# Performance work log

Measured on AMD Instinct MI355X. Metric: run time of the kernel, lower is better.

Reference implementation:

```python
import jax, jax.numpy as jnp
import numpy as np

OUTPUT_LEN = 8  # init: output_len
# init: pred_conversion=False, conf_thres=None, vote_conf_by_count=True, select_by_conf=True


def setup_inputs() -> dict:
    key = jax.random.key(0)
    x = jax.random.normal(key, (128, 8192, 64), dtype=jnp.float32)
    return {"x": x}


def _per_sample(conf, pred):
    # conf, pred: [T]
    T = conf.shape[0]
    # run-length encoding (unique_consecutive): mark the start of each run
    is_start = jnp.concatenate([jnp.ones((1,), bool), pred[1:] != pred[:-1]])
    run_id = jnp.cumsum(is_start.astype(jnp.int32)) - 1  # [T], run index per position
    # count of each run (padded to T segments; unused segments are 0)
    counts = jax.ops.segment_sum(jnp.ones((T,), conf.dtype), run_id, num_segments=T)
    # voted confidence at run starts: conf_at_start * run_count (vote_conf_by_count=True)
    voted = jnp.where(is_start, conf * counts[run_id], -jnp.inf)
    # select_by_conf=True: take top output_len runs by voted confidence
    vals, idx = jax.lax.top_k(voted, OUTPUT_LEN)
    sel = pred[idx]
    # fewer runs than output_len -> pad with 0 (torch pads with new_zeros)
    sel = jnp.where(jnp.isfinite(vals), sel, 0)
    return sel


def reference(x):
    p = jax.nn.softmax(x, axis=-1)          # [B, T, C]
    conf = jnp.max(p, axis=-1)              # [B, T]
    pred = jnp.argmax(p, axis=-1)           # [B, T] int
    out = jax.vmap(_per_sample)(conf, pred)  # [B, OUTPUT_LEN] int
    return out.astype(x.dtype)               # x.new_tensor(results) -> float
```

## Files before the change

### kernel.cpp

```cpp
#include <hip/hip_runtime.h>
#include <stdint.h>

#define T_LEN 8192
#define C_LEN 64
#define OUT_LEN 8
#define SEG 2048
#define HALO 512

__global__ __launch_bounds__(256) void softmax_stats_kernel(
    const float* __restrict__ x, int2* __restrict__ packed, int nrows)
{
    const int tid  = threadIdx.x;
    const int wave = tid >> 6;
    const int lane = tid & 63;
    const int rw   = lane >> 4;
    const int sub  = lane & 15;
    const long long row = (long long)blockIdx.x * 16 + wave * 4 + rw;
    if (row >= nrows) return;

    const float4 v = ((const float4*)(x + row * C_LEN))[sub];

    float m = v.x; int mi = sub * 4;
    if (v.y > m) { m = v.y; mi = sub * 4 + 1; }
    if (v.z > m) { m = v.z; mi = sub * 4 + 2; }
    if (v.w > m) { m = v.w; mi = sub * 4 + 3; }

    const unsigned int s0 = __float_as_uint(m);
    const unsigned int u0 = (s0 & 0x80000000u) ? ~s0 : (s0 | 0x80000000u);
    unsigned long long key =
        ((unsigned long long)u0 << 32) | (unsigned int)~mi;

    #pragma unroll
    for (int off = 8; off >= 1; off >>= 1) {
        const unsigned long long o = __shfl_xor(key, off);
        if (o > key) key = o;
    }

    const unsigned int uu = (unsigned int)(key >> 32);
    const float M = __uint_as_float(
        (uu & 0x80000000u) ? (uu ^ 0x80000000u) : ~uu);

    float s = __expf(v.x - M) + __expf(v.y - M)
            + __expf(v.z - M) + __expf(v.w - M);
    #pragma unroll
    for (int off = 8; off >= 1; off >>= 1) s += __shfl_xor(s, off);

    if (sub == 0) {
        int2 o;
        o.x = __float_as_int(1.0f / s);
        o.y = (int)~(unsigned int)(key & 0xffffffffu);
        packed[row] = o;
    }
}

__global__ __launch_bounds__(256) void topk_seg_kernel(
    const int2* __restrict__ packed, unsigned long long* __restrict__ cand)
{
    __shared__ short pred_s[SEG + HALO + 1];
    __shared__ float conf_s[SEG];
    __shared__ float voted_s[SEG];
    __shared__ unsigned long long wkey[4];
    __shared__ int dirty;

    const int tid    = threadIdx.x;
    const int lane   = tid & 63, wave = tid >> 6;
    const int sample = blockIdx.x >> 2;
    const int seg    = blockIdx.x & 3;
    const int seg_start = seg * SEG;
    const int2* __restrict__ pp = packed + (long long)sample * T_LEN;

    const int lo = (seg == 0) ? 0 : seg_start - 1;
    int hi = seg_start + SEG + HALO; if (hi > T_LEN) hi = T_LEN;
    for (int i = lo + tid; i < hi; i += 256) {
        const int2 p = pp[i];
        pred_s[i - seg_start + 1] = (short)p.y;
        const int k = i - seg_start;
        if ((unsigned)k < SEG) conf_s[k] = __int_as_float(p.x);
    }
    if (seg == 0 && tid == 0) pred_s[0] = (short)0x7fff;
    if (tid == 0) dirty = -1;
    __syncthreads();

    for (int k = tid; k < SEG; k += 256) {
        const int t = seg_start + k;
        const short p = pred_s[k + 1];
        float v = 0.0f;
        if (p != pred_s[k]) {
            int len = 1;
            const int lim = hi - t;
            while (len < lim && pred_s[k + 1 + len] == p) ++len;
            if (len == lim && t + len < T_LEN) {
                while (t + len < T_LEN && (short)pp[t + len].y == p) ++len;
            }
            v = conf_s[k] * (float)len;
        }
        voted_s[k] = v;
    }
    __syncthreads();

    for (int r = 0; r < OUT_LEN; ++r) {
        if (dirty == -1 || dirty == wave) {
            unsigned long long best = 0ull;
            const int base = wave * (SEG / 4);
            #pragma unroll
            for (int kk = 0; kk < SEG / 4 / 64; ++kk) {
                const int k = base + kk * 64 + lane;
                const unsigned long long key =
                    ((unsigned long long)__float_as_uint(voted_s[k]) << 32)
                    | (unsigned int)~(seg_start + k);
                if (key > best) best = key;
            }
            #pragma unroll
            for (int off = 32; off >= 1; off >>= 1) {
                const unsigned long long o = __shfl_xor(best, off);
                if (o > best) best = o;
            }
            if (lane == 0) wkey[wave] = best;
        }
        __syncthreads();
        if (tid == 0) {
            unsigned long long bb = wkey[0];
            #pragma unroll
            for (int w = 1; w < 4; ++w) if (wkey[w] > bb) bb = wkey[w];
            if ((bb >> 32) != 0ull) {
                const int tg = (int)~(unsigned int)(bb & 0xffffffffu);
                const int k = tg - seg_start;
                voted_s[k] = 0.0f;
                dirty = k / (SEG / 4);
            } else {
                dirty = 4;
            }
            cand[(long long)blockIdx.x * OUT_LEN + r] = bb;
        }
        __syncthreads();
    }
}

__global__ __launch_bounds__(64) void topk_merge_kernel(
    const unsigned long long* __restrict__ cand,
    const int2* __restrict__ packed, float* __restrict__ out)
{
    const int sample = blockIdx.x;
    const int lane   = threadIdx.x;

    unsigned long long key = 0ull;
    float pv = 0.0f;
    if (lane < 4 * OUT_LEN) key = cand[(long long)sample * 32 + lane];
    if (key != 0ull) {
        const int tg = (int)~(unsigned int)(key & 0xffffffffu);
        pv = (float)packed[(long long)sample * T_LEN + tg].y;
    }

    for (int r = 0; r < OUT_LEN; ++r) {
        unsigned long long best = key;
        #pragma unroll
        for (int off = 32; off >= 1; off >>= 1) {
            const unsigned long long o = __shfl_xor(best, off);
            if (o > best) best = o;
        }
        if (best == 0ull) {
            if (lane == 0) out[sample * OUT_LEN + r] = 0.0f;
        } else if (key == best) {
            out[sample * OUT_LEN + r] = pv;
            key = 0ull;
        }
    }
}

extern "C" void kernel_launch(void* const* d_in, const int* in_sizes, int n_in,
                              void* d_out, int out_size, void* d_ws, size_t ws_size,
                              hipStream_t stream) {
    const float* x  = (const float*)d_in[0];
    const int total = in_sizes[0];
    const int nrows = total / C_LEN;
    const int B     = nrows / T_LEN;

    int2* packed = (int2*)d_ws;
    unsigned long long* cand =
        (unsigned long long*)((char*)d_ws + (size_t)nrows * sizeof(int2));
    float* out = (float*)d_out;

    const int gridA = (nrows + 15) / 16;
    softmax_stats_kernel<<<gridA, 256, 0, stream>>>(x, packed, nrows);
    topk_seg_kernel<<<B * 4, 256, 0, stream>>>(packed, cand);
    topk_merge_kernel<<<B, 64, 0, stream>>>(cand, packed, out);
}
```

Baseline: 353.4 us.

## Fuse segmented top-k and merge into one per-sample kernel with register sorting networks

Replaces the two-kernel segmented top-k (4 blocks per sample, 8 serial argmax rounds with barriers, then a merge kernel) with one block of 512 threads per sample. Each thread builds 16 run-start keys, keeps its top 8 with sorting networks, and then does butterfly merges across the wave and across waves. This removes the candidate buffer, one launch, and the per-round block syncs. The cost is heavy register pressure from u64 arrays and only 128 blocks in flight, so the top-k stage has lower parallelism.

```diff
diff --git a/kernel.cpp b/kernel.cpp
--- a/kernel.cpp
+++ b/kernel.cpp
@@ -4,8 +4,7 @@
 #define T_LEN 8192
 #define C_LEN 64
 #define OUT_LEN 8
-#define SEG 2048
-#define HALO 512
+#define BTHREADS 512
 
 __global__ __launch_bounds__(256) void softmax_stats_kernel(
     const float* __restrict__ x, int2* __restrict__ packed, int nrows)
@@ -53,116 +52,112 @@
     }
 }
 
-__global__ __launch_bounds__(256) void topk_seg_kernel(
-    const int2* __restrict__ packed, unsigned long long* __restrict__ cand)
+typedef unsigned long long u64k;
+
+__device__ __forceinline__ void kcswap(u64k& a, u64k& b) {
+    if (a < b) { u64k t = a; a = b; b = t; }
+}
+
+__device__ __forceinline__ void sort8(u64k* k) {
+    kcswap(k[0],k[1]); kcswap(k[2],k[3]); kcswap(k[4],k[5]); kcswap(k[6],k[7]);
+    kcswap(k[0],k[2]); kcswap(k[1],k[3]); kcswap(k[4],k[6]); kcswap(k[5],k[7]);
+    kcswap(k[1],k[2]); kcswap(k[5],k[6]);
+    kcswap(k[0],k[4]); kcswap(k[1],k[5]); kcswap(k[2],k[6]); kcswap(k[3],k[7]);
+    kcswap(k[2],k[4]); kcswap(k[3],k[5]);
+    kcswap(k[1],k[2]); kcswap(k[3],k[4]); kcswap(k[5],k[6]);
+}
+
+__device__ __forceinline__ void merge_top8(u64k* a, const u64k* b) {
+    u64k t[8];
+    #pragma unroll
+    for (int i = 0; i < 8; ++i) {
+        const u64k x = a[i], y = b[7 - i];
+        t[i] = x > y ? x : y;
+    }
+    kcswap(t[0],t[4]); kcswap(t[1],t[5]); kcswap(t[2],t[6]); kcswap(t[3],t[7]);
+    kcswap(t[0],t[2]); kcswap(t[1],t[3]); kcswap(t[4],t[6]); kcswap(t[5],t[7]);
+    kcswap(t[0],t[1]); kcswap(t[2],t[3]); kcswap(t[4],t[5]); kcswap(t[6],t[7]);
+    #pragma unroll
+    for (int i = 0; i < 8; ++i) a[i] = t[i];
+}
+
+__global__ __launch_bounds__(BTHREADS) void topk_fused_kernel(
+    const int2* __restrict__ packed, float* __restrict__ out)
 {
-    __shared__ short pred_s[SEG + HALO + 1];
-    __shared__ float conf_s[SEG];
-    __shared__ float voted_s[SEG];
-    __shared__ unsigned long long wkey[4];
-    __shared__ int dirty;
+    __shared__ short pred_s[T_LEN];
+    __shared__ float conf_s[T_LEN];
+    __shared__ u64k  wkeys[BTHREADS / 64][OUT_LEN];
 
     const int tid    = threadIdx.x;
-    const int lane   = tid & 63, wave = tid >> 6;
-    const int sample = blockIdx.x >> 2;
-    const int seg    = blockIdx.x & 3;
-    const int seg_start = seg * SEG;
+    const int lane   = tid & 63;
+    const int wave   = tid >> 6;
+    const int sample = blockIdx.x;
     const int2* __restrict__ pp = packed + (long long)sample * T_LEN;
 
-    const int lo = (seg == 0) ? 0 : seg_start - 1;
-    int hi = seg_start + SEG + HALO; if (hi > T_LEN) hi = T_LEN;
-    for (int i = lo + tid; i < hi; i += 256) {
-        const int2 p = pp[i];
-        pred_s[i - seg_start + 1] = (short)p.y;
-        const int k = i - seg_start;
-        if ((unsigned)k < SEG) conf_s[k] = __int_as_float(p.x);
-    }
-    if (seg == 0 && tid == 0) pred_s[0] = (short)0x7fff;
-    if (tid == 0) dirty = -1;
-    __syncthreads();
-
-    for (int k = tid; k < SEG; k += 256) {
-        const int t = seg_start + k;
-        const short p = pred_s[k + 1];
-        float v = 0.0f;
-        if (p != pred_s[k]) {
-            int len = 1;
-            const int lim = hi - t;
-            while (len < lim && pred_s[k + 1 + len] == p) ++len;
-            if (len == lim && t + len < T_LEN) {
-                while (t + len < T_LEN && (short)pp[t + len].y == p) ++len;
-            }
-            v = conf_s[k] * (float)len;
-        }
-        voted_s[k] = v;
+    #pragma unroll
+    for (int i = 0; i < T_LEN / BTHREADS; ++i) {
+        const int t = tid + i * BTHREADS;
+        const int2 p = pp[t];
+        pred_s[t] = (short)p.y;
+        conf_s[t] = __int_as_float(p.x);
     }
     __syncthreads();
 
-    for (int r = 0; r < OUT_LEN; ++r) {
-        if (dirty == -1 || dirty == wave) {
-            unsigned long long best = 0ull;
-            const int base = wave * (SEG / 4);
-            #pragma unroll
-            for (int kk = 0; kk < SEG / 4 / 64; ++kk) {
-                const int k = base + kk * 64 + lane;
-                const unsigned long long key =
-                    ((unsigned long long)__float_as_uint(voted_s[k]) << 32)
-                    | (unsigned int)~(seg_start + k);
-                if (key > best) best = key;
-            }
-            #pragma unroll
-            for (int off = 32; off >= 1; off >>= 1) {
-                const unsigned long long o = __shfl_xor(best, off);
-                if (o > best) best = o;
-            }
-            if (lane == 0) wkey[wave] = best;
-        }
-        __syncthreads();
-        if (tid == 0) {
-            unsigned long long bb = wkey[0];
-            #pragma unroll
-            for (int w = 1; w < 4; ++w) if (wkey[w] > bb) bb = wkey[w];
-            if ((bb >> 32) != 0ull) {
-                const int tg = (int)~(unsigned int)(bb & 0xffffffffu);
-                const int k = tg - seg_start;
-                voted_s[k] = 0.0f;
-                dirty = k / (SEG / 4);
-            } else {
-                dirty = 4;
-            }
-            cand[(long long)blockIdx.x * OUT_LEN + r] = bb;
-        }
-        __syncthreads();
-    }
-}
+    auto make_key = [&](int t) -> u64k {
+        const short p = pred_s[t];
+        if (t != 0 && pred_s[t - 1] == p) return 0ull;
+        int len = 1;
+        while (t + len < T_LEN && pred_s[t + len] == p) ++len;
+        const float v = conf_s[t] * (float)len;
+        return ((u64k)__float_as_uint(v) << 32) | (unsigned int)~t;
+    };
 
-__global__ __launch_bounds__(64) void topk_merge_kernel(
-    const unsigned long long* __restrict__ cand,
-    const int2* __restrict__ packed, float* __restrict__ out)
-{
-    const int sample = blockIdx.x;
-    const int lane   = threadIdx.x;
+    u64k c0[8], c1[8];
+    #pragma unroll
+    for (int j = 0; j < 8; ++j) c0[j] = make_key(tid + j * BTHREADS);
+    #pragma unroll
+    for (int j = 0; j < 8; ++j) c1[j] = make_key(tid + (j + 8) * BTHREADS);
 
-    unsigned long long key = 0ull;
-    float pv = 0.0f;
-    if (lane < 4 * OUT_LEN) key = cand[(long long)sample * 32 + lane];
-    if (key != 0ull) {
-        const int tg = (int)~(unsigned int)(key & 0xffffffffu);
-        pv = (float)packed[(long long)sample * T_LEN + tg].y;
+    sort8(c0);
+    sort8(c1);
+    merge_top8(c0, c1);
+
+    #pragma unroll
+    for (int off = 1; off < 64; off <<= 1) {
+        u64k o[8];
+        #pragma unroll
+        for (int j = 0; j < 8; ++j) o[j] = __shfl_xor(c0[j], off);
+        merge_top8(c0, o);
     }
 
-    for (int r = 0; r < OUT_LEN; ++r) {
-        unsigned long long best = key;
+    if (lane == 0) {
         #pragma unroll
-        for (int off = 32; off >= 1; off >>= 1) {
-            const unsigned long long o = __shfl_xor(best, off);
-            if (o > best) best = o;
+        for (int j = 0; j < 8; ++j) wkeys[wave][j] = c0[j];
+    }
+    __syncthreads();
+
+    if (wave == 0) {
+        u64k m[8];
+        #pragma unroll
+        for (int j = 0; j < 8; ++j) m[j] = wkeys[lane & 7][j];
+        #pragma unroll
+        for (int off = 1; off < 8; off <<= 1) {
+            u64k o[8];
+            #pragma unroll
+            for (int j = 0; j < 8; ++j) o[j] = __shfl_xor(m[j], off);
+            merge_top8(m, o);
         }
-        if (best == 0ull) {
-            if (lane == 0) out[sample * OUT_LEN + r] = 0.0f;
-        } else if (key == best) {
-            out[sample * OUT_LEN + r] = pv;
-            key = 0ull;
+        if (lane == 0) {
+            #pragma unroll
+            for (int r = 0; r < OUT_LEN; ++r) {
+                const u64k key = m[r];
+                float ov = 0.0f;
+                if (key != 0ull) {
+                    const int tg = (int)~(unsigned int)(key & 0xffffffffu);
+                    ov = (float)pred_s[tg];
+                }
+                out[(long long)sample * OUT_LEN + r] = ov;
+            }
         }
     }
 }
@@ -176,12 +171,9 @@
     const int B     = nrows / T_LEN;
 
     int2* packed = (int2*)d_ws;
-    unsigned long long* cand =
-        (unsigned long long*)((char*)d_ws + (size_t)nrows * sizeof(int2));
     float* out = (float*)d_out;
 
     const int gridA = (nrows + 15) / 16;
     softmax_stats_kernel<<<gridA, 256, 0, stream>>>(x, packed, nrows);
-    topk_seg_kernel<<<B * 4, 256, 0, stream>>>(packed, cand);
-    topk_merge_kernel<<<B, 64, 0, stream>>>(cand, packed, out);
+    topk_fused_kernel<<<B, BTHREADS, 0, stream>>>(packed, out);
 }
```

New measurement: 357.8 us. No clear change (+1.2%).
